# Optimization experiments

Hardware: AMD Instinct MI355X
Metric: run time of the kernel (lower is better)

Reference implementation:

```python
import jax, jax.numpy as jnp
import numpy as np

DIM = 1024
HEADS = 16
HEAD_DIM = DIM // HEADS
B, N = 512, 65
EPS = 1e-5


def layernorm(x, w, b):
    # LayerNorm over last dim (head_dim), eps matching torch default
    mu = jnp.mean(x, axis=-1, keepdims=True)
    var = jnp.var(x, axis=-1, keepdims=True)
    return (x - mu) * jax.lax.rsqrt(var + EPS) * w + b


def setup_inputs() -> dict:
    key = jax.random.key(0)
    ks = jax.random.split(key, 8)
    s = 0.02
    return {
        "x": jax.random.normal(ks[0], (B, N, DIM), dtype=jnp.float32),
        "w_qkv": jax.random.normal(ks[1], (3 * DIM, DIM), dtype=jnp.float32) * s,
        "w_proj": jax.random.normal(ks[2], (DIM, DIM), dtype=jnp.float32) * s,
        "qn_w": jnp.ones((HEAD_DIM,), jnp.float32),
        "qn_b": jnp.zeros((HEAD_DIM,), jnp.float32),
        "kn_w": jnp.ones((HEAD_DIM,), jnp.float32),
        "kn_b": jnp.zeros((HEAD_DIM,), jnp.float32),
        "bias": jax.random.normal(ks[3], (HEADS, 65, 65), dtype=jnp.float32) * 0.1,
        "bias_scale": jnp.array(1.0, jnp.float32),
    }


def reference(x, w_qkv, w_proj, qn_w, qn_b, kn_w, kn_b, bias, bias_scale):
    Bsz, n, C = x.shape
    scale = HEAD_DIM ** -0.5
    qkv = jnp.einsum('bnc,dc->bnd', x, w_qkv)              # [B,N,3C]
    qkv = qkv.reshape(Bsz, n, 3, HEADS, HEAD_DIM)
    qkv = jnp.transpose(qkv, (2, 0, 3, 1, 4))              # [3,B,H,N,hd]
    q, k, v = qkv[0], qkv[1], qkv[2]
    q = layernorm(q, qn_w, qn_b) * scale
    k = layernorm(k, kn_w, kn_b)
    attn = jnp.einsum('bhnd,bhmd->bhnm', q, k)             # [B,H,N,N]
    attn = attn + (bias[:, :n, :n] * bias_scale)[None]
    attn = jax.nn.softmax(attn, axis=-1)
    out = jnp.einsum('bhnm,bhmd->bhnd', attn, v)           # [B,H,N,hd]
    out = jnp.transpose(out, (0, 2, 1, 3)).reshape(Bsz, n, C)
    return jnp.einsum('bnc,dc->bnd', out, w_proj)
```

## Files before the change

kernel.cpp:

```cpp
#include <hip/hip_runtime.h>
#include <stdint.h>

#define HEADS 16
#define BSZ 512
#define NTOK 65
#define MTOK (BSZ * NTOK)
#define NX  34078720UL
#define NQW 3145728UL
#define NPW 1048576UL

typedef __attribute__((ext_vector_type(8))) short bf16x8;
typedef __attribute__((ext_vector_type(4))) float f32x4;

__device__ __forceinline__ unsigned short f2bf(float f) {
  unsigned u = __float_as_uint(f);
  u += 0x7FFFu + ((u >> 16) & 1u);
  return (unsigned short)(u >> 16);
}

__global__ __launch_bounds__(256) void cast3_kernel(
    const float* __restrict__ x, const float* __restrict__ wq, const float* __restrict__ wp,
    unsigned short* __restrict__ xb, unsigned short* __restrict__ wqb, unsigned short* __restrict__ wpb) {
  size_t u = ((size_t)blockIdx.x * 256 + threadIdx.x) * 4;
  const float* src; unsigned short* dst; size_t off;
  if (u < NX)            { src = x;  dst = xb;  off = u; }
  else if (u < NX + NQW) { src = wq; dst = wqb; off = u - NX; }
  else                   { src = wp; dst = wpb; off = u - NX - NQW; }
  float4 v = *(const float4*)(src + off);
  ushort4 o;
  o.x = f2bf(v.x); o.y = f2bf(v.y); o.z = f2bf(v.z); o.w = f2bf(v.w);
  *(ushort4*)(dst + off) = o;
}

template <int MODE>
__global__ __launch_bounds__(256) void gemm_bt_kernel(
    const unsigned short* __restrict__ A, const unsigned short* __restrict__ Bm,
    unsigned short* __restrict__ qws, unsigned short* __restrict__ kws,
    unsigned short* __restrict__ vws, float* __restrict__ outp,
    const float* __restrict__ qn_w, const float* __restrict__ qn_b,
    const float* __restrict__ kn_w, const float* __restrict__ kn_b) {
  __shared__ unsigned short As[128 * 64];
  __shared__ unsigned short Bs[128 * 64];
  const int tid = threadIdx.x;
  const int wid = tid >> 6, lane = tid & 63;
  const int lrow = lane & 15, lk = lane >> 4;
  const int bm = blockIdx.y, bn = blockIdx.x;
  const int wr = (wid >> 1) * 64, wc = (wid & 1) * 64;
  const size_t arow0 = (size_t)bm * 128, brow0 = (size_t)bn * 128;

  f32x4 acc[4][4] = {};

  for (int kt = 0; kt < 16; ++kt) {
    __syncthreads();
    const int k0 = kt * 64;
#pragma unroll
    for (int j = 0; j < 4; ++j) {
      int ci = j * 256 + tid;
      int row = ci >> 3, k8s = ci & 7;
      int k8 = k8s ^ (row & 7);
      const unsigned short* srcA = A + (arow0 + row) * 1024 + k0 + k8 * 8;
      __builtin_amdgcn_global_load_lds(
          (const __attribute__((address_space(1))) unsigned int*)srcA,
          (__attribute__((address_space(3))) unsigned int*)As + (size_t)(j * 256 + wid * 64) * 4,
          16, 0, 0);
      const unsigned short* srcB = Bm + (brow0 + row) * 1024 + k0 + k8 * 8;
      __builtin_amdgcn_global_load_lds(
          (const __attribute__((address_space(1))) unsigned int*)srcB,
          (__attribute__((address_space(3))) unsigned int*)Bs + (size_t)(j * 256 + wid * 64) * 4,
          16, 0, 0);
    }
    __syncthreads();
#pragma unroll
    for (int kk = 0; kk < 2; ++kk) {
      const int cpos = (kk * 4 + lk) ^ (lrow & 7);
      bf16x8 af[4], bfv[4];
#pragma unroll
      for (int mt = 0; mt < 4; ++mt)
        af[mt] = *(const bf16x8*)&As[(wr + mt * 16 + lrow) * 64 + cpos * 8];
#pragma unroll
      for (int nt = 0; nt < 4; ++nt)
        bfv[nt] = *(const bf16x8*)&Bs[(wc + nt * 16 + lrow) * 64 + cpos * 8];
#pragma unroll
      for (int mt = 0; mt < 4; ++mt)
#pragma unroll
        for (int nt = 0; nt < 4; ++nt)
          acc[mt][nt] = __builtin_amdgcn_mfma_f32_16x16x32_bf16(af[mt], bfv[nt], acc[mt][nt], 0, 0, 0);
    }
  }

  if (MODE == 0) {
    const int sec = bn >> 3;
    const int h0 = ((bn & 7) << 1) + (wc >> 6);
    const float qsc = (sec == 0) ? 0.125f : 1.0f;
    float wv[4], bvv[4];
    if (sec < 2) {
      const float* wp_ = sec ? kn_w : qn_w;
      const float* bp_ = sec ? kn_b : qn_b;
#pragma unroll
      for (int nt = 0; nt < 4; ++nt) {
        wv[nt] = wp_[nt * 16 + lrow];
        bvv[nt] = bp_[nt * 16 + lrow];
      }
    }
    unsigned short* qk_dst = sec ? kws : qws;
#pragma unroll
    for (int mt = 0; mt < 4; ++mt)
#pragma unroll
      for (int r = 0; r < 4; ++r) {
        int grow = bm * 128 + wr + mt * 16 + lk * 4 + r;
        int b = grow / 65, nn = grow - b * 65;
        int bh = b * HEADS + h0;
        if (sec < 2) {
          float s = 0.f, s2 = 0.f;
#pragma unroll
          for (int nt = 0; nt < 4; ++nt) {
            float f = acc[mt][nt][r];
            s += f; s2 += f * f;
          }
          s += __shfl_xor(s, 1); s2 += __shfl_xor(s2, 1);
          s += __shfl_xor(s, 2); s2 += __shfl_xor(s2, 2);
          s += __shfl_xor(s, 4); s2 += __shfl_xor(s2, 4);
          s += __shfl_xor(s, 8); s2 += __shfl_xor(s2, 8);
          float mu = s * 0.015625f;
          float rstd = rsqrtf(s2 * 0.015625f - mu * mu + 1e-5f);
          size_t base = ((size_t)bh * 65 + nn) * 64;
#pragma unroll
          for (int nt = 0; nt < 4; ++nt)
            qk_dst[base + nt * 16 + lrow] =
                f2bf(((acc[mt][nt][r] - mu) * rstd * wv[nt] + bvv[nt]) * qsc);
        } else {
#pragma unroll
          for (int nt = 0; nt < 4; ++nt)
            vws[((size_t)bh * 64 + nt * 16 + lrow) * 80 + nn] = f2bf(acc[mt][nt][r]);
        }
      }
  } else {
    const size_t cb = (size_t)bn * 128 + wc + lrow;
#pragma unroll
    for (int mt = 0; mt < 4; ++mt)
#pragma unroll
      for (int r = 0; r < 4; ++r) {
        float* rp = outp + (size_t)(bm * 128 + wr + mt * 16 + lk * 4 + r) * 1024 + cb;
#pragma unroll
        for (int nt = 0; nt < 4; ++nt) rp[nt * 16] = acc[mt][nt][r];
      }
  }
}

__global__ __launch_bounds__(256, 4) void attn_kernel(
    const unsigned short* __restrict__ qws, const unsigned short* __restrict__ kws,
    const unsigned short* __restrict__ vws,
    const float* __restrict__ bias, const float* __restrict__ bias_scale,
    unsigned short* __restrict__ aws) {
  __shared__ unsigned short qk_s[2 * 80 * 64];
  __shared__ unsigned short v_s[64 * 128];
  const int tid = threadIdx.x;
  const int wid = tid >> 6;
  const int bh = blockIdx.x;
  const int b = bh >> 4, h = bh & 15;
  const size_t qbase = (size_t)bh * 65 * 64;
  const size_t vbase = (size_t)bh * 64 * 80;

#pragma unroll
  for (int it = 0; it < 2; ++it) {
    int ci = it * 256 + tid;
    int row = ci >> 3, k8s = ci & 7;
    int k8 = k8s ^ (row & 7);
    __builtin_amdgcn_global_load_lds(
        (const __attribute__((address_space(1))) unsigned int*)(qws + qbase + row * 64 + k8 * 8),
        (__attribute__((address_space(3))) unsigned int*)qk_s + (size_t)(it * 256 + wid * 64) * 4,
        16, 0, 0);
    __builtin_amdgcn_global_load_lds(
        (const __attribute__((address_space(1))) unsigned int*)(kws + qbase + row * 64 + k8 * 8),
        (__attribute__((address_space(3))) unsigned int*)qk_s + (size_t)(640 + it * 256 + wid * 64) * 4,
        16, 0, 0);
  }
  if (tid < 8) {
    bf16x8 tq = *(const bf16x8*)&qws[qbase + 64 * 64 + tid * 8];
    *(bf16x8*)&qk_s[64 * 64 + tid * 8] = tq;
  } else if (tid < 16) {
    int t = tid - 8;
    bf16x8 tk = *(const bf16x8*)&kws[qbase + 64 * 64 + t * 8];
    *(bf16x8*)&qk_s[5120 + 64 * 64 + t * 8] = tk;
  }
#pragma unroll
  for (int it = 0; it < 4; ++it) {
    int ci = it * 256 + tid;
    int d = ci >> 4, cs = ci & 15;
    int c = cs ^ (d & 7);
    __builtin_amdgcn_global_load_lds(
        (const __attribute__((address_space(1))) unsigned int*)(vws + vbase + d * 80 + c * 8),
        (__attribute__((address_space(3))) unsigned int*)v_s + (size_t)(it * 256 + wid * 64) * 4,
        16, 0, 0);
  }
  __syncthreads();

  const int lane = tid & 63;
  const int lrow = lane & 15, lk = lane >> 4;
  const float bsc = *bias_scale;
  const unsigned short* q_s = qk_s;
  const unsigned short* k_s = qk_s + 5120;
  unsigned short* p_s = qk_s;

  auto qkt_softmax = [&](int s, unsigned int (&pk)[5][2]) {
    f32x4 accs[5] = {};
#pragma unroll
    for (int kk = 0; kk < 2; ++kk) {
      const int cpos = (kk * 4 + lk) ^ (lrow & 7);
      bf16x8 af = *(const bf16x8*)&q_s[(s * 16 + lrow) * 64 + cpos * 8];
#pragma unroll
      for (int nt = 0; nt < 5; ++nt) {
        bf16x8 bv = *(const bf16x8*)&k_s[(nt * 16 + lrow) * 64 + cpos * 8];
        accs[nt] = __builtin_amdgcn_mfma_f32_16x16x32_bf16(af, bv, accs[nt], 0, 0, 0);
      }
    }
#pragma unroll
    for (int r = 0; r < 4; ++r) {
      int row = s * 16 + lk * 4 + r;
      int brow = row > 64 ? 64 : row;
      float vals[5];
#pragma unroll
      for (int nt = 0; nt < 5; ++nt) {
        int col = nt * 16 + lrow;
        float v = accs[nt][r];
        if (col < 65) v += bias[((size_t)h * 65 + brow) * 65 + col] * bsc;
        else v = -1e30f;
        vals[nt] = v;
      }
      float m = vals[0];
#pragma unroll
      for (int nt = 1; nt < 5; ++nt) m = fmaxf(m, vals[nt]);
      m = fmaxf(m, __shfl_xor(m, 1)); m = fmaxf(m, __shfl_xor(m, 2));
      m = fmaxf(m, __shfl_xor(m, 4)); m = fmaxf(m, __shfl_xor(m, 8));
      float ssum = 0.f;
#pragma unroll
      for (int nt = 0; nt < 5; ++nt) { vals[nt] = __expf(vals[nt] - m); ssum += vals[nt]; }
      ssum += __shfl_xor(ssum, 1); ssum += __shfl_xor(ssum, 2);
      ssum += __shfl_xor(ssum, 4); ssum += __shfl_xor(ssum, 8);
      float inv = 1.0f / ssum;
#pragma unroll
      for (int nt = 0; nt < 5; ++nt) {
        unsigned int u = (unsigned int)f2bf(vals[nt] * inv);
        if ((r & 1) == 0) pk[nt][r >> 1] = u;
        else pk[nt][r >> 1] |= u << 16;
      }
    }
  };

  auto pwrite = [&](int s, const unsigned int (&pk)[5][2]) {
#pragma unroll
    for (int r = 0; r < 4; ++r) {
      int row = s * 16 + lk * 4 + r;
#pragma unroll
      for (int nt = 0; nt < 5; ++nt) {
        int col = nt * 16 + lrow;
        p_s[row * 128 + ((col >> 3) ^ (row & 7)) * 8 + (col & 7)] =
            (unsigned short)(pk[nt][r >> 1] >> ((r & 1) * 16));
      }
#pragma unroll
      for (int nt = 5; nt < 8; ++nt) {
        int col = nt * 16 + lrow;
        p_s[row * 128 + ((col >> 3) ^ (row & 7)) * 8 + (col & 7)] = 0;
      }
    }
  };

  unsigned int pk0[5][2], pk1[5][2];
  qkt_softmax(wid, pk0);
  if (wid == 0) qkt_softmax(4, pk1);
  __syncthreads();
  pwrite(wid, pk0);
  if (wid == 0) pwrite(4, pk1);
  __syncthreads();

  const size_t obase = (size_t)b * 65 * 1024 + h * 64;
  for (int s = wid; s < 5; s += 4) {
    f32x4 acco[4] = {};
#pragma unroll
    for (int kk = 0; kk < 3; ++kk) {
      const int cpos = (kk * 4 + lk) ^ (lrow & 7);
      bf16x8 af = *(const bf16x8*)&p_s[(s * 16 + lrow) * 128 + cpos * 8];
#pragma unroll
      for (int nt = 0; nt < 4; ++nt) {
        bf16x8 bv = *(const bf16x8*)&v_s[(nt * 16 + lrow) * 128 + cpos * 8];
        acco[nt] = __builtin_amdgcn_mfma_f32_16x16x32_bf16(af, bv, acco[nt], 0, 0, 0);
      }
    }
#pragma unroll
    for (int r = 0; r < 4; ++r) {
      int row = s * 16 + lk * 4 + r;
      if (row < 65) {
#pragma unroll
        for (int nt = 0; nt < 4; ++nt)
          aws[obase + (size_t)row * 1024 + nt * 16 + lrow] = f2bf(acco[nt][r]);
      }
    }
  }
}

extern "C" void kernel_launch(void* const* d_in, const int* in_sizes, int n_in,
                              void* d_out, int out_size, void* d_ws, size_t ws_size,
                              hipStream_t stream) {
  const float* x     = (const float*)d_in[0];
  const float* wqkv  = (const float*)d_in[1];
  const float* wproj = (const float*)d_in[2];
  const float* qn_w  = (const float*)d_in[3];
  const float* qn_b  = (const float*)d_in[4];
  const float* kn_w  = (const float*)d_in[5];
  const float* kn_b  = (const float*)d_in[6];
  const float* bias  = (const float*)d_in[7];
  const float* bsc   = (const float*)d_in[8];
  float* out = (float*)d_out;

  unsigned short* xb  = (unsigned short*)d_ws;
  unsigned short* wqb = xb + NX;
  unsigned short* wpb = wqb + NQW;
  unsigned short* qws = wpb + NPW;
  unsigned short* kws = qws + 34078720UL;
  unsigned short* vws = kws + 34078720UL;
  unsigned short* aws = vws + 41943040UL;

  cast3_kernel<<<37376, 256, 0, stream>>>(x, wqkv, wproj, xb, wqb, wpb);
  gemm_bt_kernel<0><<<dim3(24, 260), 256, 0, stream>>>(xb, wqb, qws, kws, vws, nullptr,
                                                       qn_w, qn_b, kn_w, kn_b);
  attn_kernel<<<8192, 256, 0, stream>>>(qws, kws, vws, bias, bsc, aws);
  gemm_bt_kernel<1><<<dim3(8, 260), 256, 0, stream>>>(aws, wpb, nullptr, nullptr, nullptr, out,
                                                      nullptr, nullptr, nullptr, nullptr);
}
```

Measured before the change: 799.4 us.

## Replace QKV GEMM with 256x256 tile double-buffered direct-to-LDS kernel

```diff
diff --git a/kernel.cpp b/kernel.cpp
--- a/kernel.cpp
+++ b/kernel.cpp
@@ -30,6 +30,143 @@
   ushort4 o;
   o.x = f2bf(v.x); o.y = f2bf(v.y); o.z = f2bf(v.z); o.w = f2bf(v.w);
   *(ushort4*)(dst + off) = o;
+}
+
+__global__ __launch_bounds__(512, 2) void gemm0_256_kernel(
+    const unsigned short* __restrict__ A, const unsigned short* __restrict__ Bm,
+    unsigned short* __restrict__ qws, unsigned short* __restrict__ kws,
+    unsigned short* __restrict__ vws,
+    const float* __restrict__ qn_w, const float* __restrict__ qn_b,
+    const float* __restrict__ kn_w, const float* __restrict__ kn_b) {
+  __shared__ unsigned short As0[256 * 64];
+  __shared__ unsigned short Bs0[256 * 64];
+  __shared__ unsigned short As1[256 * 64];
+  __shared__ unsigned short Bs1[256 * 64];
+  const int tid = threadIdx.x;
+  const int wid = tid >> 6, lane = tid & 63;
+  const int lrow = lane & 15, lk = lane >> 4;
+  const int wm = wid >> 2, wn = wid & 3;
+
+  const int orig = blockIdx.x;
+  const int wg = (orig & 7) * 195 + (orig >> 3);
+  const int bm = wg / 12, bn = wg - bm * 12;
+
+  const size_t arow0 = (size_t)bm * 256, brow0 = (size_t)bn * 256;
+
+  const unsigned short* pA[4];
+  const unsigned short* pB[4];
+  int dstc[4];
+#pragma unroll
+  for (int j = 0; j < 4; ++j) {
+    int ci = j * 512 + tid;
+    int row = ci >> 3;
+    int k8 = (ci & 7) ^ (row & 7);
+    pA[j] = A + (arow0 + row) * 1024 + k8 * 8;
+    pB[j] = Bm + (brow0 + row) * 1024 + k8 * 8;
+    dstc[j] = (j * 512 + wid * 64) * 4;
+  }
+
+  f32x4 acc[2][4][4] = {};
+
+  auto stage = [&](unsigned short* __restrict__ dA, unsigned short* __restrict__ dB, int ktn) {
+    const int koff = ktn * 64;
+#pragma unroll
+    for (int j = 0; j < 4; ++j) {
+      __builtin_amdgcn_global_load_lds(
+          (const __attribute__((address_space(1))) unsigned int*)(pA[j] + koff),
+          (__attribute__((address_space(3))) unsigned int*)dA + dstc[j], 16, 0, 0);
+      __builtin_amdgcn_global_load_lds(
+          (const __attribute__((address_space(1))) unsigned int*)(pB[j] + koff),
+          (__attribute__((address_space(3))) unsigned int*)dB + dstc[j], 16, 0, 0);
+    }
+  };
+
+  auto ktile = [&](const unsigned short* __restrict__ RA, const unsigned short* __restrict__ RB,
+                   unsigned short* __restrict__ WA, unsigned short* __restrict__ WB, int ktn) {
+    if (ktn < 16) stage(WA, WB, ktn);
+#pragma unroll
+    for (int kk = 0; kk < 2; ++kk) {
+      const int cpos8 = ((kk * 4 + lk) ^ (lrow & 7)) * 8;
+      bf16x8 bv[4];
+#pragma unroll
+      for (int nt = 0; nt < 4; ++nt)
+        bv[nt] = *(const bf16x8*)&RB[(wn * 64 + nt * 16 + lrow) * 64 + cpos8];
+#pragma unroll
+      for (int mh = 0; mh < 2; ++mh) {
+        bf16x8 av[4];
+#pragma unroll
+        for (int mt = 0; mt < 4; ++mt)
+          av[mt] = *(const bf16x8*)&RA[(wm * 128 + mh * 64 + mt * 16 + lrow) * 64 + cpos8];
+        __builtin_amdgcn_s_barrier();
+        __builtin_amdgcn_s_setprio(1);
+#pragma unroll
+        for (int mt = 0; mt < 4; ++mt)
+#pragma unroll
+          for (int nt = 0; nt < 4; ++nt)
+            acc[mh][mt][nt] =
+                __builtin_amdgcn_mfma_f32_16x16x32_bf16(av[mt], bv[nt], acc[mh][mt][nt], 0, 0, 0);
+        __builtin_amdgcn_s_setprio(0);
+      }
+    }
+    __syncthreads();
+  };
+
+  stage(As0, Bs0, 0);
+  __syncthreads();
+
+#pragma unroll 1
+  for (int kt2 = 0; kt2 < 8; ++kt2) {
+    ktile(As0, Bs0, As1, Bs1, 2 * kt2 + 1);
+    ktile(As1, Bs1, As0, Bs0, 2 * kt2 + 2);
+  }
+
+  const int sec = bn >> 2;
+  const int h0 = ((bn & 3) << 2) + wn;
+  const float qsc = (sec == 0) ? 0.125f : 1.0f;
+  float wv[4], bvv[4];
+  if (sec < 2) {
+    const float* wp_ = sec ? kn_w : qn_w;
+    const float* bp_ = sec ? kn_b : qn_b;
+#pragma unroll
+    for (int nt = 0; nt < 4; ++nt) {
+      wv[nt] = wp_[nt * 16 + lrow];
+      bvv[nt] = bp_[nt * 16 + lrow];
+    }
+  }
+  unsigned short* qk_dst = sec ? kws : qws;
+#pragma unroll
+  for (int mh = 0; mh < 2; ++mh)
+#pragma unroll
+    for (int mt = 0; mt < 4; ++mt)
+#pragma unroll
+      for (int r = 0; r < 4; ++r) {
+        int grow = bm * 256 + wm * 128 + mh * 64 + mt * 16 + lk * 4 + r;
+        int b = grow / 65, nn = grow - b * 65;
+        int bh = b * HEADS + h0;
+        if (sec < 2) {
+          float s = 0.f, s2 = 0.f;
+#pragma unroll
+          for (int nt = 0; nt < 4; ++nt) {
+            float f = acc[mh][mt][nt][r];
+            s += f; s2 += f * f;
+          }
+          s += __shfl_xor(s, 1); s2 += __shfl_xor(s2, 1);
+          s += __shfl_xor(s, 2); s2 += __shfl_xor(s2, 2);
+          s += __shfl_xor(s, 4); s2 += __shfl_xor(s2, 4);
+          s += __shfl_xor(s, 8); s2 += __shfl_xor(s2, 8);
+          float mu = s * 0.015625f;
+          float rstd = rsqrtf(s2 * 0.015625f - mu * mu + 1e-5f);
+          size_t base = ((size_t)bh * 65 + nn) * 64;
+#pragma unroll
+          for (int nt = 0; nt < 4; ++nt)
+            qk_dst[base + nt * 16 + lrow] =
+                f2bf(((acc[mh][mt][nt][r] - mu) * rstd * wv[nt] + bvv[nt]) * qsc);
+        } else {
+#pragma unroll
+          for (int nt = 0; nt < 4; ++nt)
+            vws[((size_t)bh * 64 + nt * 16 + lrow) * 80 + nn] = f2bf(acc[mh][mt][nt][r]);
+        }
+      }
 }
 
 template <int MODE>
@@ -89,51 +226,6 @@
   }
 
   if (MODE == 0) {
-    const int sec = bn >> 3;
-    const int h0 = ((bn & 7) << 1) + (wc >> 6);
-    const float qsc = (sec == 0) ? 0.125f : 1.0f;
-    float wv[4], bvv[4];
-    if (sec < 2) {
-      const float* wp_ = sec ? kn_w : qn_w;
-      const float* bp_ = sec ? kn_b : qn_b;
-#pragma unroll
-      for (int nt = 0; nt < 4; ++nt) {
-        wv[nt] = wp_[nt * 16 + lrow];
-        bvv[nt] = bp_[nt * 16 + lrow];
-      }
-    }
-    unsigned short* qk_dst = sec ? kws : qws;
-#pragma unroll
-    for (int mt = 0; mt < 4; ++mt)
-#pragma unroll
-      for (int r = 0; r < 4; ++r) {
-        int grow = bm * 128 + wr + mt * 16 + lk * 4 + r;
-        int b = grow / 65, nn = grow - b * 65;
-        int bh = b * HEADS + h0;
-        if (sec < 2) {
-          float s = 0.f, s2 = 0.f;
-#pragma unroll
-          for (int nt = 0; nt < 4; ++nt) {
-            float f = acc[mt][nt][r];
-            s += f; s2 += f * f;
-          }
-          s += __shfl_xor(s, 1); s2 += __shfl_xor(s2, 1);
-          s += __shfl_xor(s, 2); s2 += __shfl_xor(s2, 2);
-          s += __shfl_xor(s, 4); s2 += __shfl_xor(s2, 4);
-          s += __shfl_xor(s, 8); s2 += __shfl_xor(s2, 8);
-          float mu = s * 0.015625f;
-          float rstd = rsqrtf(s2 * 0.015625f - mu * mu + 1e-5f);
-          size_t base = ((size_t)bh * 65 + nn) * 64;
-#pragma unroll
-          for (int nt = 0; nt < 4; ++nt)
-            qk_dst[base + nt * 16 + lrow] =
-                f2bf(((acc[mt][nt][r] - mu) * rstd * wv[nt] + bvv[nt]) * qsc);
-        } else {
-#pragma unroll
-          for (int nt = 0; nt < 4; ++nt)
-            vws[((size_t)bh * 64 + nt * 16 + lrow) * 80 + nn] = f2bf(acc[mt][nt][r]);
-        }
-      }
   } else {
     const size_t cb = (size_t)bn * 128 + wc + lrow;
 #pragma unroll
@@ -321,8 +413,8 @@
   unsigned short* aws = vws + 41943040UL;
 
   cast3_kernel<<<37376, 256, 0, stream>>>(x, wqkv, wproj, xb, wqb, wpb);
-  gemm_bt_kernel<0><<<dim3(24, 260), 256, 0, stream>>>(xb, wqb, qws, kws, vws, nullptr,
-                                                       qn_w, qn_b, kn_w, kn_b);
+  gemm0_256_kernel<<<1560, 512, 0, stream>>>(xb, wqb, qws, kws, vws,
+                                             qn_w, qn_b, kn_w, kn_b);
   attn_kernel<<<8192, 256, 0, stream>>>(qws, kws, vws, bias, bsc, aws);
   gemm_bt_kernel<1><<<dim3(8, 260), 256, 0, stream>>>(aws, wpb, nullptr, nullptr, nullptr, out,
                                                       nullptr, nullptr, nullptr, nullptr);
```

New measurement: 741.3 us. 1.08x faster.
